# Kernel tuning notes

Measured on AMD Instinct MI355X. Metric: run time of the kernel, lower is better.

## Reference

```python
import jax, jax.numpy as jnp
import numpy as np

H = 32          # num_attention_heads
ROPE_BASE = 10000.0


def _rotary_freqs_cis(seq_len: int, head_dim: int) -> jnp.ndarray:
    # complex e^{i * pos * theta_j}, shape [seq_len, head_dim//2]
    inv_freq = 1.0 / (ROPE_BASE ** (jnp.arange(0, head_dim, 2, dtype=jnp.float32) / head_dim))
    angles = jnp.arange(seq_len, dtype=jnp.float32)[:, None] * inv_freq[None, :]
    return jax.lax.complex(jnp.cos(angles), jnp.sin(angles))


def _apply_rotary(u: jnp.ndarray, freqs_cis: jnp.ndarray) -> jnp.ndarray:
    # u: [B, S, H, hd]; faithful to apply_rotary_emb (interleaved pairs -> complex mul)
    ur = u.astype(jnp.float32).reshape(*u.shape[:-1], -1, 2)
    uc = jax.lax.complex(ur[..., 0], ur[..., 1])
    # freqs_cis broadcast: [1, S, 1, hd//2]
    uc = uc * freqs_cis[None, :, None, :]
    return jnp.stack((jnp.real(uc), jnp.imag(uc)), axis=-1).reshape(u.shape)


def setup_inputs() -> dict:
    key = jax.random.key(0)
    ks = jax.random.split(key, 5)
    B, S, D = 1, 2048, 4096
    init_std = 0.02
    x = jax.random.normal(ks[0], (B, S, D), dtype=jnp.float32)
    wq = jax.random.normal(ks[1], (D, D), dtype=jnp.float32) * init_std
    wk = jax.random.normal(ks[2], (D, D), dtype=jnp.float32) * init_std
    wv = jax.random.normal(ks[3], (D, D), dtype=jnp.float32) * init_std
    wo = jax.random.normal(ks[4], (D, D), dtype=jnp.float32) * init_std
    return {"x": x, "wq": wq, "wk": wk, "wv": wv, "wo": wo}


def reference(x, wq, wk, wv, wo):
    B, S, D = x.shape
    hd = D // H  # head_dim = 128
    q = (x @ wq).reshape(B, S, H, hd)
    k = (x @ wk).reshape(B, S, H, hd)
    v = (x @ wv).reshape(B, S, H, hd)

    freqs_cis = _rotary_freqs_cis(S, hd)
    q = _apply_rotary(q, freqs_cis)
    k = _apply_rotary(k, freqs_cis)
    # n_rep == 1 (num_key_value_heads == num_attention_heads) -> repeat_kv is identity

    scale = 1.0 / jnp.sqrt(jnp.float32(hd))
    scores = jnp.einsum('bqhd,bkhd->bhqk', q, k) * scale  # [B, H, S, S]
    causal = jnp.tril(jnp.ones((S, S), dtype=bool))
    neg = jnp.finfo(scores.dtype).min
    scores = jnp.where(causal[None, None, :, :], scores, neg)
    probs = jax.nn.softmax(scores, axis=-1)
    attn = jnp.einsum('bhqk,bkhd->bqhd', probs, v).reshape(B, S, D)
    return attn @ wo
```

## Files before the change

kernel.cpp:

```cpp
#include <hip/hip_runtime.h>
#include <stdint.h>

#define S_LEN 2048
#define DMODEL 4096
#define NHEAD 32
#define HDIM 128

typedef __attribute__((ext_vector_type(8))) short bf16x8;
typedef __attribute__((ext_vector_type(4))) float f32x4;

__device__ __forceinline__ unsigned short f2bf(float f) {
    union { float f; unsigned u; } v; v.f = f;
    unsigned u = v.u;
    unsigned r = (u + 0x7FFFu + ((u >> 16) & 1u)) >> 16;
    return (unsigned short)r;
}
__device__ __forceinline__ float bf2f(unsigned short h) {
    union { unsigned u; float f; } v; v.u = ((unsigned)h) << 16;
    return v.f;
}

__global__ void convert_x_kernel(const float* __restrict__ x,
                                 unsigned short* __restrict__ xb, int n4) {
    int t = blockIdx.x * blockDim.x + threadIdx.x;
    if (t >= n4) return;
    float4 v = ((const float4*)x)[t];
    ushort4 o;
    o.x = f2bf(v.x); o.y = f2bf(v.y); o.z = f2bf(v.z); o.w = f2bf(v.w);
    ((ushort4*)xb)[t] = o;
}

__global__ void convert_wt_kernel(const float* __restrict__ w,
                                  unsigned short* __restrict__ wt) {
    __shared__ unsigned short t[64][65];
    int n0 = blockIdx.x * 64, k0 = blockIdx.y * 64;
    for (int i = 0; i < 16; ++i) {
        int o = threadIdx.x + i * 256;
        int r = o >> 6, c = o & 63;
        t[r][c] = f2bf(w[(size_t)(k0 + r) * DMODEL + n0 + c]);
    }
    __syncthreads();
    for (int i = 0; i < 16; ++i) {
        int o = threadIdx.x + i * 256;
        int rr = o >> 6, kk = o & 63;
        wt[(size_t)(n0 + rr) * DMODEL + k0 + kk] = t[kk][rr];
    }
}


#define MFMA16(a, b, c) __builtin_amdgcn_mfma_f32_16x16x32_bf16(a, b, c, 0, 0, 0)

#define GLDS(g, l) __builtin_amdgcn_global_load_lds( \
    (__attribute__((address_space(1))) unsigned int*)(g), \
    (__attribute__((address_space(3))) unsigned int*)(l), 16, 0, 0)

#define VMCNT_(n) asm volatile("s_waitcnt vmcnt(" #n ")" ::: "memory")
#define VMCNT(n) VMCNT_(n)

#define PH_SYNC() \
    __builtin_amdgcn_sched_barrier(0); \
    __builtin_amdgcn_s_barrier(); \
    asm volatile("s_waitcnt lgkmcnt(0)" ::: "memory"); \
    __builtin_amdgcn_sched_barrier(0)

#define PH_END() \
    __builtin_amdgcn_s_setprio(0); \
    __builtin_amdgcn_sched_barrier(0); \
    __builtin_amdgcn_s_barrier(); \
    __builtin_amdgcn_sched_barrier(0)

#define PH_END_VM(VM) \
    __builtin_amdgcn_s_setprio(0); \
    __builtin_amdgcn_sched_barrier(0); \
    VMCNT(VM); \
    __builtin_amdgcn_s_barrier(); \
    __builtin_amdgcn_sched_barrier(0)

#define STAGE_A(T, PAR, J) do { \
    size_t ko_ = (size_t)(T) * 64 + (J) * 32; \
    GLDS(gA0 + ko_, As + ((PAR) * 2 + (J)) * 8192 + w * 512); \
    GLDS(gA1 + ko_, As + ((PAR) * 2 + (J)) * 8192 + 4096 + w * 512); \
} while (0)
#define STAGE_B(T, PAR, J) do { \
    size_t ko_ = (size_t)(T) * 64 + (J) * 32; \
    GLDS(gB + ko_, Bs + ((PAR) * 2 + (J)) * 4096 + w * 512); \
} while (0)

#define TILE(T, P, S1, S2, VM2, VM4) do { \
    const unsigned short* AsT = As + (P) * 16384; \
    const unsigned short* BsT = Bs + (P) * 8192; \
    bf16x8 af0, af1, af2, af3, bf0, bf1, bf2, bf3; \
    af0 = *(const bf16x8*)&AsT[offA0]; \
    af1 = *(const bf16x8*)&AsT[offA1]; \
    af2 = *(const bf16x8*)&AsT[offA2]; \
    af3 = *(const bf16x8*)&AsT[offA3]; \
    bf0 = *(const bf16x8*)&BsT[offB0]; \
    bf1 = *(const bf16x8*)&BsT[offB1]; \
    if (S1) STAGE_A((T) + 1, (P) ^ 1, 1); \
    PH_SYNC(); \
    __builtin_amdgcn_s_setprio(1); \
    acc[0][0] = MFMA16(af0, bf0, acc[0][0]); \
    acc[1][0] = MFMA16(af1, bf0, acc[1][0]); \
    acc[2][0] = MFMA16(af2, bf0, acc[2][0]); \
    acc[3][0] = MFMA16(af3, bf0, acc[3][0]); \
    acc[0][1] = MFMA16(af0, bf1, acc[0][1]); \
    acc[1][1] = MFMA16(af1, bf1, acc[1][1]); \
    acc[2][1] = MFMA16(af2, bf1, acc[2][1]); \
    acc[3][1] = MFMA16(af3, bf1, acc[3][1]); \
    PH_END(); \
    bf2 = *(const bf16x8*)&BsT[offB2]; \
    bf3 = *(const bf16x8*)&BsT[offB3]; \
    if (S1) STAGE_B((T) + 1, (P) ^ 1, 1); \
    PH_SYNC(); \
    __builtin_amdgcn_s_setprio(1); \
    acc[0][2] = MFMA16(af0, bf2, acc[0][2]); \
    acc[1][2] = MFMA16(af1, bf2, acc[1][2]); \
    acc[2][2] = MFMA16(af2, bf2, acc[2][2]); \
    acc[3][2] = MFMA16(af3, bf2, acc[3][2]); \
    acc[0][3] = MFMA16(af0, bf3, acc[0][3]); \
    acc[1][3] = MFMA16(af1, bf3, acc[1][3]); \
    acc[2][3] = MFMA16(af2, bf3, acc[2][3]); \
    acc[3][3] = MFMA16(af3, bf3, acc[3][3]); \
    PH_END_VM(VM2); \
    af0 = *(const bf16x8*)&AsT[8192 + offA0]; \
    af1 = *(const bf16x8*)&AsT[8192 + offA1]; \
    af2 = *(const bf16x8*)&AsT[8192 + offA2]; \
    af3 = *(const bf16x8*)&AsT[8192 + offA3]; \
    bf0 = *(const bf16x8*)&BsT[4096 + offB0]; \
    bf1 = *(const bf16x8*)&BsT[4096 + offB1]; \
    if (S2) STAGE_A((T) + 2, (P), 0); \
    PH_SYNC(); \
    __builtin_amdgcn_s_setprio(1); \
    acc[0][0] = MFMA16(af0, bf0, acc[0][0]); \
    acc[1][0] = MFMA16(af1, bf0, acc[1][0]); \
    acc[2][0] = MFMA16(af2, bf0, acc[2][0]); \
    acc[3][0] = MFMA16(af3, bf0, acc[3][0]); \
    acc[0][1] = MFMA16(af0, bf1, acc[0][1]); \
    acc[1][1] = MFMA16(af1, bf1, acc[1][1]); \
    acc[2][1] = MFMA16(af2, bf1, acc[2][1]); \
    acc[3][1] = MFMA16(af3, bf1, acc[3][1]); \
    PH_END(); \
    bf2 = *(const bf16x8*)&BsT[4096 + offB2]; \
    bf3 = *(const bf16x8*)&BsT[4096 + offB3]; \
    if (S2) STAGE_B((T) + 2, (P), 0); \
    PH_SYNC(); \
    __builtin_amdgcn_s_setprio(1); \
    acc[0][2] = MFMA16(af0, bf2, acc[0][2]); \
    acc[1][2] = MFMA16(af1, bf2, acc[1][2]); \
    acc[2][2] = MFMA16(af2, bf2, acc[2][2]); \
    acc[3][2] = MFMA16(af3, bf2, acc[3][2]); \
    acc[0][3] = MFMA16(af0, bf3, acc[0][3]); \
    acc[1][3] = MFMA16(af1, bf3, acc[1][3]); \
    acc[2][3] = MFMA16(af2, bf3, acc[2][3]); \
    acc[3][3] = MFMA16(af3, bf3, acc[3][3]); \
    PH_END_VM(VM4); \
} while (0)

template<int STORE_MODE>
__global__ __launch_bounds__(512, 2)
void gemm8p_kernel(const unsigned short* __restrict__ A,
                   const unsigned short* __restrict__ BT,
                   void* __restrict__ C) {
    constexpr int M = S_LEN, N = DMODEL, K = DMODEL;
    constexpr int NT = K / 64;
    extern __shared__ __align__(16) unsigned short sm[];
    unsigned short* As = sm;
    unsigned short* Bs = sm + 32768;

    const int tid = threadIdx.x;
    const int lane = tid & 63;
    const int w = tid >> 6;
    const int wr = w >> 1, wc = w & 1;
    const int q = lane >> 4, lm = lane & 15;

    int orig = blockIdx.y * gridDim.x + blockIdx.x;
    const int by = orig & 7;
    const int bx = orig >> 3;
    const int m0 = by * 256, n0 = bx * 128;

    const int c4 = tid & 3, r4 = tid >> 2, s4 = (tid >> 3) & 3;
    const unsigned short* gA0 = A + (size_t)(m0 + r4) * K + ((c4 ^ s4) * 8);
    const unsigned short* gA1 = gA0 + (size_t)128 * K;
    const unsigned short* gB  = BT + (size_t)(n0 + r4) * K + ((c4 ^ s4) * 8);

#define FRAGOFF(r_) ((r_) * 32 + ((q ^ (((r_) >> 1) & 3)) * 8))
    const int rA = wr * 64 + lm, rB = wc * 64 + lm;
    const int offA0 = FRAGOFF(rA);
    const int offA1 = FRAGOFF(rA + 16);
    const int offA2 = FRAGOFF(rA + 32);
    const int offA3 = FRAGOFF(rA + 48);
    const int offB0 = FRAGOFF(rB);
    const int offB1 = FRAGOFF(rB + 16);
    const int offB2 = FRAGOFF(rB + 32);
    const int offB3 = FRAGOFF(rB + 48);
#undef FRAGOFF

    f32x4 zero = {0.f, 0.f, 0.f, 0.f};
    f32x4 acc[4][4];
    for (int i = 0; i < 4; ++i)
        for (int j = 0; j < 4; ++j) acc[i][j] = zero;

    STAGE_A(0, 0, 0); STAGE_B(0, 0, 0);
    STAGE_A(0, 0, 1); STAGE_B(0, 0, 1);
    STAGE_A(1, 1, 0); STAGE_B(1, 1, 0);
    VMCNT(6);
    __builtin_amdgcn_s_barrier();
    __builtin_amdgcn_sched_barrier(0);

    for (int t = 0; t < NT - 2; t += 2) {
        TILE(t, 0, true, true, 6, 6);
        TILE(t + 1, 1, true, true, 6, 6);
    }
    TILE(NT - 2, 0, true, false, 6, 3);
    TILE(NT - 1, 1, false, false, 0, 0);

    for (int mi = 0; mi < 4; ++mi) {
        int mbase = m0 + wr * 64 + mi * 16 + q * 4;
        for (int ni = 0; ni < 4; ++ni) {
            int n = n0 + wc * 64 + ni * 16 + lm;
            if (STORE_MODE == 0) {
                unsigned short* Cb = (unsigned short*)C;
                for (int r = 0; r < 4; ++r)
                    Cb[(size_t)(mbase + r) * N + n] = f2bf(acc[mi][ni][r]);
            } else if (STORE_MODE == 1) {
                unsigned short* Cb = (unsigned short*)C;
                ushort4 v;
                v.x = f2bf(acc[mi][ni][0]); v.y = f2bf(acc[mi][ni][1]);
                v.z = f2bf(acc[mi][ni][2]); v.w = f2bf(acc[mi][ni][3]);
                *(ushort4*)&Cb[(size_t)n * M + mbase] = v;
            } else {
                float* Cf = (float*)C;
                for (int r = 0; r < 4; ++r)
                    Cf[(size_t)(mbase + r) * N + n] = acc[mi][ni][r];
            }
        }
    }
}

__global__ void rope_kernel(unsigned short* __restrict__ qb,
                            unsigned short* __restrict__ kb) {
    int t = blockIdx.x * blockDim.x + threadIdx.x;
    if (t >= S_LEN * DMODEL / 2) return;
    int s = t >> 11;
    int p = t & 2047;
    int j = p & 63;
    float ang = (float)s * exp2f((float)j * -0.2076205059304602f);
    float sn, cs;
    sincosf(ang, &sn, &cs);
    size_t idx = (size_t)s * DMODEL + 2 * p;
    const float SC = 0.08838834764831845f;
    float a0 = bf2f(qb[idx]), a1 = bf2f(qb[idx + 1]);
    qb[idx]     = f2bf((a0 * cs - a1 * sn) * SC);
    qb[idx + 1] = f2bf((a0 * sn + a1 * cs) * SC);
    float b0 = bf2f(kb[idx]), b1 = bf2f(kb[idx + 1]);
    kb[idx]     = f2bf(b0 * cs - b1 * sn);
    kb[idx + 1] = f2bf(b0 * sn + b1 * cs);
}

__global__ __launch_bounds__(256, 2)
void attn_kernel(const unsigned short* __restrict__ qb,
                 const unsigned short* __restrict__ kb,
                 const unsigned short* __restrict__ vt,
                 unsigned short* __restrict__ ab) {
    __shared__ __align__(16) unsigned short Ks[64 * 128];
    __shared__ __align__(16) unsigned short VTs[128 * 64];
    __shared__ __align__(16) unsigned short Pb[4][32 * 72];
    const int t = threadIdx.x;
    const int lane = t & 63;
    const int w = t >> 6;
    const int h = blockIdx.y;
    const int q0 = ((int)gridDim.x - 1 - (int)blockIdx.x) * 128;
    const int qw = q0 + w * 32;
    const int q = lane >> 4, lm = lane & 15;

    const int krow = t >> 2;
    const int kcol = t & 3;
    const int vrow = t >> 1;
    const int vcol = t & 1;

    const unsigned short* gK = kb + (size_t)krow * DMODEL + h * HDIM;
    const unsigned short* gV = vt + (size_t)(h * HDIM + vrow) * S_LEN;

    bf16x8 qf[2][4];
#pragma unroll
    for (int qt = 0; qt < 2; ++qt)
#pragma unroll
        for (int kc = 0; kc < 4; ++kc)
            qf[qt][kc] = *(const bf16x8*)&qb[(size_t)(qw + qt * 16 + lm) * DMODEL
                                            + h * HDIM + kc * 32 + q * 8];

    f32x4 zero = {0.f, 0.f, 0.f, 0.f};
    f32x4 o[2][8];
#pragma unroll
    for (int qt = 0; qt < 2; ++qt)
        for (int i = 0; i < 8; ++i) o[qt][i] = zero;
    float mrow[2][4], lrow[2][4];
#pragma unroll
    for (int qt = 0; qt < 2; ++qt)
        for (int r = 0; r < 4; ++r) { mrow[qt][r] = -1e30f; lrow[qt][r] = 0.f; }

    const int nch = q0 / 64 + 2;

    bf16x8 kreg[4], vreg[4];
#pragma unroll
    for (int i = 0; i < 4; ++i) {
        kreg[i] = *(const bf16x8*)&gK[(size_t)0 * DMODEL + (kcol + i * 4) * 8];
        vreg[i] = *(const bf16x8*)&gV[0 + (vcol + i * 2) * 8];
    }
#pragma unroll
    for (int i = 0; i < 4; ++i) {
        *(bf16x8*)&Ks[krow * 128 + (((kcol + i * 4) ^ (krow & 15)) * 8)] = kreg[i];
        *(bf16x8*)&VTs[vrow * 64 + (((vcol + i * 2) ^ (vrow & 7)) * 8)] = vreg[i];
    }
    __syncthreads();

    for (int c = 0; c < nch; ++c) {
        const int j0 = c * 64;
        if (c + 1 < nch) {
            const size_t jn = (size_t)(j0 + 64);
#pragma unroll
            for (int i = 0; i < 4; ++i) {
                kreg[i] = *(const bf16x8*)&gK[jn * DMODEL + (kcol + i * 4) * 8];
                vreg[i] = *(const bf16x8*)&gV[jn + (vcol + i * 2) * 8];
            }
        }

        if (j0 <= qw + 31) {
            f32x4 s[2][4];
#pragma unroll
            for (int qt = 0; qt < 2; ++qt)
                for (int ks = 0; ks < 4; ++ks) s[qt][ks] = zero;
#pragma unroll
            for (int kc = 0; kc < 4; ++kc)
#pragma unroll
                for (int ks = 0; ks < 4; ++ks) {
                    bf16x8 kf = *(const bf16x8*)&Ks[(ks * 16 + lm) * 128
                                                    + (((kc * 4 + q) ^ lm) * 8)];
                    s[0][ks] = __builtin_amdgcn_mfma_f32_16x16x32_bf16(qf[0][kc], kf, s[0][ks], 0, 0, 0);
                    s[1][ks] = __builtin_amdgcn_mfma_f32_16x16x32_bf16(qf[1][kc], kf, s[1][ks], 0, 0, 0);
                }
            if (j0 + 63 > qw) {
#pragma unroll
                for (int qt = 0; qt < 2; ++qt)
#pragma unroll
                    for (int ks = 0; ks < 4; ++ks)
#pragma unroll
                        for (int r = 0; r < 4; ++r)
                            if (j0 + ks * 16 + lm > qw + qt * 16 + q * 4 + r)
                                s[qt][ks][r] = -1e30f;
            }

            float mx[2][4];
#pragma unroll
            for (int qt = 0; qt < 2; ++qt)
#pragma unroll
                for (int r = 0; r < 4; ++r)
                    mx[qt][r] = fmaxf(fmaxf(s[qt][0][r], s[qt][1][r]),
                                      fmaxf(s[qt][2][r], s[qt][3][r]));
#pragma unroll
            for (int st = 1; st <= 8; st <<= 1)
#pragma unroll
                for (int qt = 0; qt < 2; ++qt)
#pragma unroll
                    for (int r = 0; r < 4; ++r)
                        mx[qt][r] = fmaxf(mx[qt][r], __shfl_xor(mx[qt][r], st));

            float aln[2][4], mnv[2][4], rs[2][4];
#pragma unroll
            for (int qt = 0; qt < 2; ++qt)
#pragma unroll
                for (int r = 0; r < 4; ++r) {
                    mnv[qt][r] = fmaxf(mrow[qt][r], mx[qt][r]);
                    aln[qt][r] = __expf(mrow[qt][r] - mnv[qt][r]);
                    mrow[qt][r] = mnv[qt][r];
                }
#pragma unroll
            for (int qt = 0; qt < 2; ++qt)
#pragma unroll
                for (int ks = 0; ks < 4; ++ks)
#pragma unroll
                    for (int r = 0; r < 4; ++r)
                        s[qt][ks][r] = __expf(s[qt][ks][r] - mnv[qt][r]);
#pragma unroll
            for (int qt = 0; qt < 2; ++qt)
#pragma unroll
                for (int r = 0; r < 4; ++r)
                    rs[qt][r] = (s[qt][0][r] + s[qt][1][r]) + (s[qt][2][r] + s[qt][3][r]);
#pragma unroll
            for (int st = 1; st <= 8; st <<= 1)
#pragma unroll
                for (int qt = 0; qt < 2; ++qt)
#pragma unroll
                    for (int r = 0; r < 4; ++r)
                        rs[qt][r] += __shfl_xor(rs[qt][r], st);
#pragma unroll
            for (int qt = 0; qt < 2; ++qt)
#pragma unroll
                for (int r = 0; r < 4; ++r)
                    lrow[qt][r] = lrow[qt][r] * aln[qt][r] + rs[qt][r];

#pragma unroll
            for (int qt = 0; qt < 2; ++qt)
#pragma unroll
                for (int ks = 0; ks < 4; ++ks)
#pragma unroll
                    for (int r = 0; r < 4; ++r)
                        Pb[w][(qt * 16 + q * 4 + r) * 72 + ks * 16 + lm] = f2bf(s[qt][ks][r]);

            bf16x8 pA[2][2];
#pragma unroll
            for (int qt = 0; qt < 2; ++qt) {
                pA[qt][0] = *(const bf16x8*)&Pb[w][(qt * 16 + lm) * 72 + q * 8];
                pA[qt][1] = *(const bf16x8*)&Pb[w][(qt * 16 + lm) * 72 + 32 + q * 8];
            }
#pragma unroll
            for (int nt = 0; nt < 8; ++nt) {
                int d = nt * 16 + lm;
                bf16x8 vf0 = *(const bf16x8*)&VTs[d * 64 + ((q ^ (d & 7)) * 8)];
                bf16x8 vf1 = *(const bf16x8*)&VTs[d * 64 + (((4 + q) ^ (d & 7)) * 8)];
#pragma unroll
                for (int qt = 0; qt < 2; ++qt) {
                    f32x4 oo = o[qt][nt];
#pragma unroll
                    for (int r = 0; r < 4; ++r) oo[r] *= aln[qt][r];
                    oo = __builtin_amdgcn_mfma_f32_16x16x32_bf16(pA[qt][0], vf0, oo, 0, 0, 0);
                    o[qt][nt] = __builtin_amdgcn_mfma_f32_16x16x32_bf16(pA[qt][1], vf1, oo, 0, 0, 0);
                }
            }
        }

        __syncthreads();
        if (c + 1 < nch) {
#pragma unroll
            for (int i = 0; i < 4; ++i) {
                *(bf16x8*)&Ks[krow * 128 + (((kcol + i * 4) ^ (krow & 15)) * 8)] = kreg[i];
                *(bf16x8*)&VTs[vrow * 64 + (((vcol + i * 2) ^ (vrow & 7)) * 8)] = vreg[i];
            }
        }
        __syncthreads();
    }

    float inv[2][4];
#pragma unroll
    for (int qt = 0; qt < 2; ++qt)
#pragma unroll
        for (int r = 0; r < 4; ++r) inv[qt][r] = 1.0f / lrow[qt][r];
#pragma unroll
    for (int qt = 0; qt < 2; ++qt)
#pragma unroll
        for (int nt = 0; nt < 8; ++nt) {
            int d = h * HDIM + lm + nt * 16;
#pragma unroll
            for (int r = 0; r < 4; ++r)
                ab[(size_t)(qw + qt * 16 + q * 4 + r) * DMODEL + d] =
                    f2bf(o[qt][nt][r] * inv[qt][r]);
        }
}

extern "C" void kernel_launch(void* const* d_in, const int* in_sizes, int n_in,
                              void* d_out, int out_size, void* d_ws, size_t ws_size,
                              hipStream_t stream) {
    const float* x  = (const float*)d_in[0];
    const float* wq = (const float*)d_in[1];
    const float* wk = (const float*)d_in[2];
    const float* wv = (const float*)d_in[3];
    const float* wo = (const float*)d_in[4];
    char* ws = (char*)d_ws;
    const size_t MB = 1024 * 1024;
    unsigned short* xb  = (unsigned short*)(ws + 0 * MB);
    unsigned short* qb  = (unsigned short*)(ws + 16 * MB);
    unsigned short* kb  = (unsigned short*)(ws + 32 * MB);
    unsigned short* vtb = (unsigned short*)(ws + 48 * MB);
    unsigned short* ab  = (unsigned short*)(ws + 64 * MB);
    unsigned short* wtb = (unsigned short*)(ws + 80 * MB);

    static int attr_done = 0;
    if (!attr_done) {
        hipFuncSetAttribute((const void*)&gemm8p_kernel<0>,
                            hipFuncAttributeMaxDynamicSharedMemorySize, 98304);
        hipFuncSetAttribute((const void*)&gemm8p_kernel<1>,
                            hipFuncAttributeMaxDynamicSharedMemorySize, 98304);
        hipFuncSetAttribute((const void*)&gemm8p_kernel<2>,
                            hipFuncAttributeMaxDynamicSharedMemorySize, 98304);
        attr_done = 1;
    }

    dim3 cg(64, 64);
    dim3 gg(32, 8);

    convert_x_kernel<<<(S_LEN * DMODEL / 4) / 256, 256, 0, stream>>>(x, xb, S_LEN * DMODEL / 4);

    convert_wt_kernel<<<cg, 256, 0, stream>>>(wq, wtb);
    gemm8p_kernel<0><<<gg, 512, 98304, stream>>>(xb, wtb, qb);
    convert_wt_kernel<<<cg, 256, 0, stream>>>(wk, wtb);
    gemm8p_kernel<0><<<gg, 512, 98304, stream>>>(xb, wtb, kb);
    convert_wt_kernel<<<cg, 256, 0, stream>>>(wv, wtb);
    gemm8p_kernel<1><<<gg, 512, 98304, stream>>>(xb, wtb, vtb);

    rope_kernel<<<(S_LEN * DMODEL / 2) / 256, 256, 0, stream>>>(qb, kb);

    attn_kernel<<<dim3(S_LEN / 128, NHEAD), 256, 0, stream>>>(qb, kb, vtb, ab);

    convert_wt_kernel<<<cg, 256, 0, stream>>>(wo, wtb);
    gemm8p_kernel<2><<<gg, 512, 98304, stream>>>(ab, wtb, d_out);
}
```

Before: 721.9 us.

## Restructure attention inner loop with async K staging and register-shuffled P

The attention kernel now double-buffers K tiles in shared memory, filled with direct global-to-LDS loads (GLDS) so the next tile streams in while the current one is computed, and one barrier per chunk replaces the two __syncthreads. V is read straight from global memory into registers instead of going through LDS. The QK^T MFMA operands are swapped so each lane holds a transposed score tile, which makes row max and row sum reductions need only two cross-lane shuffles. P is packed to bf16 with v_cvt_pk_bf16_f32 and rearranged into MFMA operand layout with lane shuffles instead of an LDS round trip. The cost is more shuffle traffic and uncached global V loads issued on every chunk.

New measurement: 744.1 us. 3.1% more time.

```diff
diff --git a/kernel.cpp b/kernel.cpp
--- a/kernel.cpp
+++ b/kernel.cpp
@@ -262,9 +262,7 @@
                  const unsigned short* __restrict__ kb,
                  const unsigned short* __restrict__ vt,
                  unsigned short* __restrict__ ab) {
-    __shared__ __align__(16) unsigned short Ks[64 * 128];
-    __shared__ __align__(16) unsigned short VTs[128 * 64];
-    __shared__ __align__(16) unsigned short Pb[4][32 * 72];
+    __shared__ __align__(16) unsigned short Ks[2][64 * 128];
     const int t = threadIdx.x;
     const int lane = t & 63;
     const int w = t >> 6;
@@ -272,14 +270,18 @@
     const int q0 = ((int)gridDim.x - 1 - (int)blockIdx.x) * 128;
     const int qw = q0 + w * 32;
     const int q = lane >> 4, lm = lane & 15;
-
-    const int krow = t >> 2;
-    const int kcol = t & 3;
-    const int vrow = t >> 1;
-    const int vcol = t & 1;
-
-    const unsigned short* gK = kb + (size_t)krow * DMODEL + h * HDIM;
-    const unsigned short* gV = vt + (size_t)(h * HDIM + vrow) * S_LEN;
+    const int w16 = w * 16;
+
+#define ATT_STAGE(CHUNK, BUF) do { \
+    size_t rbase_ = (size_t)((CHUNK) * 64); \
+    _Pragma("unroll") \
+    for (int j_ = 0; j_ < 4; ++j_) { \
+        int rloc_ = w16 + j_ * 4 + (lane >> 4); \
+        const unsigned short* src_ = kb + (rbase_ + rloc_) * DMODEL + h * HDIM \
+                                     + (((lane & 15) ^ (rloc_ & 15)) * 8); \
+        GLDS(src_, &Ks[BUF][(w16 + j_ * 4) * 128]); \
+    } \
+} while (0)
 
     bf16x8 qf[2][4];
 #pragma unroll
@@ -294,38 +296,31 @@
 #pragma unroll
     for (int qt = 0; qt < 2; ++qt)
         for (int i = 0; i < 8; ++i) o[qt][i] = zero;
-    float mrow[2][4], lrow[2][4];
-#pragma unroll
-    for (int qt = 0; qt < 2; ++qt)
-        for (int r = 0; r < 4; ++r) { mrow[qt][r] = -1e30f; lrow[qt][r] = 0.f; }
+    float mrow[2] = {-1e30f, -1e30f};
+    float lrow[2] = {0.f, 0.f};
 
     const int nch = q0 / 64 + 2;
 
-    bf16x8 kreg[4], vreg[4];
-#pragma unroll
-    for (int i = 0; i < 4; ++i) {
-        kreg[i] = *(const bf16x8*)&gK[(size_t)0 * DMODEL + (kcol + i * 4) * 8];
-        vreg[i] = *(const bf16x8*)&gV[0 + (vcol + i * 2) * 8];
-    }
-#pragma unroll
-    for (int i = 0; i < 4; ++i) {
-        *(bf16x8*)&Ks[krow * 128 + (((kcol + i * 4) ^ (krow & 15)) * 8)] = kreg[i];
-        *(bf16x8*)&VTs[vrow * 64 + (((vcol + i * 2) ^ (vrow & 7)) * 8)] = vreg[i];
-    }
-    __syncthreads();
+    ATT_STAGE(0, 0);
+    VMCNT(0);
+    __builtin_amdgcn_s_barrier();
+    __builtin_amdgcn_sched_barrier(0);
 
     for (int c = 0; c < nch; ++c) {
         const int j0 = c * 64;
-        if (c + 1 < nch) {
-            const size_t jn = (size_t)(j0 + 64);
-#pragma unroll
-            for (int i = 0; i < 4; ++i) {
-                kreg[i] = *(const bf16x8*)&gK[jn * DMODEL + (kcol + i * 4) * 8];
-                vreg[i] = *(const bf16x8*)&gV[jn + (vcol + i * 2) * 8];
+        const int p = c & 1;
+        if (c + 1 < nch) ATT_STAGE(c + 1, p ^ 1);
+
+        if (j0 <= qw + 31) {
+            bf16x8 vf0[8], vf1[8];
+#pragma unroll
+            for (int nt = 0; nt < 8; ++nt) {
+                const unsigned short* gv = vt + (size_t)(h * HDIM + nt * 16 + lm) * S_LEN
+                                           + j0 + q * 8;
+                vf0[nt] = *(const bf16x8*)gv;
+                vf1[nt] = *(const bf16x8*)(gv + 32);
             }
-        }
-
-        if (j0 <= qw + 31) {
+
             f32x4 s[2][4];
 #pragma unroll
             for (int qt = 0; qt < 2; ++qt)
@@ -334,10 +329,10 @@
             for (int kc = 0; kc < 4; ++kc)
 #pragma unroll
                 for (int ks = 0; ks < 4; ++ks) {
-                    bf16x8 kf = *(const bf16x8*)&Ks[(ks * 16 + lm) * 128
-                                                    + (((kc * 4 + q) ^ lm) * 8)];
-                    s[0][ks] = __builtin_amdgcn_mfma_f32_16x16x32_bf16(qf[0][kc], kf, s[0][ks], 0, 0, 0);
-                    s[1][ks] = __builtin_amdgcn_mfma_f32_16x16x32_bf16(qf[1][kc], kf, s[1][ks], 0, 0, 0);
+                    bf16x8 kf = *(const bf16x8*)&Ks[p][(ks * 16 + lm) * 128
+                                                      + (((kc * 4 + q) ^ lm) * 8)];
+                    s[0][ks] = __builtin_amdgcn_mfma_f32_16x16x32_bf16(kf, qf[0][kc], s[0][ks], 0, 0, 0);
+                    s[1][ks] = __builtin_amdgcn_mfma_f32_16x16x32_bf16(kf, qf[1][kc], s[1][ks], 0, 0, 0);
                 }
             if (j0 + 63 > qw) {
 #pragma unroll
@@ -346,105 +341,108 @@
                     for (int ks = 0; ks < 4; ++ks)
 #pragma unroll
                         for (int r = 0; r < 4; ++r)
-                            if (j0 + ks * 16 + lm > qw + qt * 16 + q * 4 + r)
+                            if (j0 + ks * 16 + q * 4 + r > qw + qt * 16 + lm)
                                 s[qt][ks][r] = -1e30f;
             }
 
-            float mx[2][4];
+            float alnv[2];
+#pragma unroll
+            for (int qt = 0; qt < 2; ++qt) {
+                float m01 = fmaxf(fmaxf(s[qt][0][0], s[qt][0][1]), fmaxf(s[qt][0][2], s[qt][0][3]));
+                float m11 = fmaxf(fmaxf(s[qt][1][0], s[qt][1][1]), fmaxf(s[qt][1][2], s[qt][1][3]));
+                float m21 = fmaxf(fmaxf(s[qt][2][0], s[qt][2][1]), fmaxf(s[qt][2][2], s[qt][2][3]));
+                float m31 = fmaxf(fmaxf(s[qt][3][0], s[qt][3][1]), fmaxf(s[qt][3][2], s[qt][3][3]));
+                float mloc = fmaxf(fmaxf(m01, m11), fmaxf(m21, m31));
+                mloc = fmaxf(mloc, __shfl_xor(mloc, 16));
+                mloc = fmaxf(mloc, __shfl_xor(mloc, 32));
+                float mn = fmaxf(mrow[qt], mloc);
+                alnv[qt] = __expf(mrow[qt] - mn);
+                mrow[qt] = mn;
+#pragma unroll
+                for (int ks = 0; ks < 4; ++ks)
+#pragma unroll
+                    for (int r = 0; r < 4; ++r)
+                        s[qt][ks][r] = __expf(s[qt][ks][r] - mn);
+                float r0 = (s[qt][0][0] + s[qt][0][1]) + (s[qt][0][2] + s[qt][0][3]);
+                float r1 = (s[qt][1][0] + s[qt][1][1]) + (s[qt][1][2] + s[qt][1][3]);
+                float r2 = (s[qt][2][0] + s[qt][2][1]) + (s[qt][2][2] + s[qt][2][3]);
+                float r3 = (s[qt][3][0] + s[qt][3][1]) + (s[qt][3][2] + s[qt][3][3]);
+                float rloc = (r0 + r1) + (r2 + r3);
+                rloc += __shfl_xor(rloc, 16);
+                rloc += __shfl_xor(rloc, 32);
+                lrow[qt] = lrow[qt] * alnv[qt] + rloc;
+            }
+
+            unsigned Wd[2][4][2];
 #pragma unroll
             for (int qt = 0; qt < 2; ++qt)
 #pragma unroll
+                for (int ks = 0; ks < 4; ++ks)
+#pragma unroll
+                    for (int u = 0; u < 2; ++u) {
+                        unsigned wv;
+                        asm("v_cvt_pk_bf16_f32 %0, %1, %2"
+                            : "=v"(wv) : "v"(s[qt][ks][2 * u]), "v"(s[qt][ks][2 * u + 1]));
+                        Wd[qt][ks][u] = wv;
+                    }
+
+            union U8 { bf16x8 v; unsigned u[4]; };
+            const int sA = ((lane >> 4) & 1) * 32 + lm;
+            const int sB = sA + 16;
+            const bool hi2 = (lane & 32) != 0;
+            U8 pA[2][2];
+#pragma unroll
+            for (int qt = 0; qt < 2; ++qt)
+#pragma unroll
+                for (int hh = 0; hh < 2; ++hh) {
+                    unsigned a0 = __shfl((int)Wd[qt][2 * hh][0], sA);
+                    unsigned b0 = __shfl((int)Wd[qt][2 * hh + 1][0], sA);
+                    pA[qt][hh].u[0] = hi2 ? b0 : a0;
+                    unsigned a1 = __shfl((int)Wd[qt][2 * hh][1], sA);
+                    unsigned b1 = __shfl((int)Wd[qt][2 * hh + 1][1], sA);
+                    pA[qt][hh].u[1] = hi2 ? b1 : a1;
+                    unsigned a2 = __shfl((int)Wd[qt][2 * hh][0], sB);
+                    unsigned b2 = __shfl((int)Wd[qt][2 * hh + 1][0], sB);
+                    pA[qt][hh].u[2] = hi2 ? b2 : a2;
+                    unsigned a3 = __shfl((int)Wd[qt][2 * hh][1], sB);
+                    unsigned b3 = __shfl((int)Wd[qt][2 * hh + 1][1], sB);
+                    pA[qt][hh].u[3] = hi2 ? b3 : a3;
+                }
+
+            float alno[2][4];
+#pragma unroll
+            for (int qt = 0; qt < 2; ++qt)
+#pragma unroll
                 for (int r = 0; r < 4; ++r)
-                    mx[qt][r] = fmaxf(fmaxf(s[qt][0][r], s[qt][1][r]),
-                                      fmaxf(s[qt][2][r], s[qt][3][r]));
-#pragma unroll
-            for (int st = 1; st <= 8; st <<= 1)
-#pragma unroll
-                for (int qt = 0; qt < 2; ++qt)
-#pragma unroll
-                    for (int r = 0; r < 4; ++r)
-                        mx[qt][r] = fmaxf(mx[qt][r], __shfl_xor(mx[qt][r], st));
-
-            float aln[2][4], mnv[2][4], rs[2][4];
-#pragma unroll
-            for (int qt = 0; qt < 2; ++qt)
-#pragma unroll
-                for (int r = 0; r < 4; ++r) {
-                    mnv[qt][r] = fmaxf(mrow[qt][r], mx[qt][r]);
-                    aln[qt][r] = __expf(mrow[qt][r] - mnv[qt][r]);
-                    mrow[qt][r] = mnv[qt][r];
-                }
-#pragma unroll
-            for (int qt = 0; qt < 2; ++qt)
-#pragma unroll
-                for (int ks = 0; ks < 4; ++ks)
-#pragma unroll
-                    for (int r = 0; r < 4; ++r)
-                        s[qt][ks][r] = __expf(s[qt][ks][r] - mnv[qt][r]);
-#pragma unroll
-            for (int qt = 0; qt < 2; ++qt)
-#pragma unroll
-                for (int r = 0; r < 4; ++r)
-                    rs[qt][r] = (s[qt][0][r] + s[qt][1][r]) + (s[qt][2][r] + s[qt][3][r]);
-#pragma unroll
-            for (int st = 1; st <= 8; st <<= 1)
-#pragma unroll
-                for (int qt = 0; qt < 2; ++qt)
-#pragma unroll
-                    for (int r = 0; r < 4; ++r)
-                        rs[qt][r] += __shfl_xor(rs[qt][r], st);
-#pragma unroll
-            for (int qt = 0; qt < 2; ++qt)
-#pragma unroll
-                for (int r = 0; r < 4; ++r)
-                    lrow[qt][r] = lrow[qt][r] * aln[qt][r] + rs[qt][r];
-
-#pragma unroll
-            for (int qt = 0; qt < 2; ++qt)
-#pragma unroll
-                for (int ks = 0; ks < 4; ++ks)
-#pragma unroll
-                    for (int r = 0; r < 4; ++r)
-                        Pb[w][(qt * 16 + q * 4 + r) * 72 + ks * 16 + lm] = f2bf(s[qt][ks][r]);
-
-            bf16x8 pA[2][2];
-#pragma unroll
-            for (int qt = 0; qt < 2; ++qt) {
-                pA[qt][0] = *(const bf16x8*)&Pb[w][(qt * 16 + lm) * 72 + q * 8];
-                pA[qt][1] = *(const bf16x8*)&Pb[w][(qt * 16 + lm) * 72 + 32 + q * 8];
-            }
+                    alno[qt][r] = __shfl(alnv[qt], (lane >> 4) * 4 + r);
+
 #pragma unroll
             for (int nt = 0; nt < 8; ++nt) {
-                int d = nt * 16 + lm;
-                bf16x8 vf0 = *(const bf16x8*)&VTs[d * 64 + ((q ^ (d & 7)) * 8)];
-                bf16x8 vf1 = *(const bf16x8*)&VTs[d * 64 + (((4 + q) ^ (d & 7)) * 8)];
 #pragma unroll
                 for (int qt = 0; qt < 2; ++qt) {
                     f32x4 oo = o[qt][nt];
 #pragma unroll
-                    for (int r = 0; r < 4; ++r) oo[r] *= aln[qt][r];
-                    oo = __builtin_amdgcn_mfma_f32_16x16x32_bf16(pA[qt][0], vf0, oo, 0, 0, 0);
-                    o[qt][nt] = __builtin_amdgcn_mfma_f32_16x16x32_bf16(pA[qt][1], vf1, oo, 0, 0, 0);
+                    for (int r = 0; r < 4; ++r) oo[r] *= alno[qt][r];
+                    oo = __builtin_amdgcn_mfma_f32_16x16x32_bf16(pA[qt][0].v, vf0[nt], oo, 0, 0, 0);
+                    o[qt][nt] = __builtin_amdgcn_mfma_f32_16x16x32_bf16(pA[qt][1].v, vf1[nt], oo, 0, 0, 0);
                 }
             }
         }
 
-        __syncthreads();
-        if (c + 1 < nch) {
-#pragma unroll
-            for (int i = 0; i < 4; ++i) {
-                *(bf16x8*)&Ks[krow * 128 + (((kcol + i * 4) ^ (krow & 15)) * 8)] = kreg[i];
-                *(bf16x8*)&VTs[vrow * 64 + (((vcol + i * 2) ^ (vrow & 7)) * 8)] = vreg[i];
-            }
-        }
-        __syncthreads();
-    }
-
-    float inv[2][4];
-#pragma unroll
-    for (int qt = 0; qt < 2; ++qt)
-#pragma unroll
-        for (int r = 0; r < 4; ++r) inv[qt][r] = 1.0f / lrow[qt][r];
+        __builtin_amdgcn_sched_barrier(0);
+        VMCNT(0);
+        __builtin_amdgcn_s_barrier();
+        __builtin_amdgcn_sched_barrier(0);
+    }
+
+    float invo[2][4];
+#pragma unroll
+    for (int qt = 0; qt < 2; ++qt) {
+        float iv = 1.0f / lrow[qt];
+#pragma unroll
+        for (int r = 0; r < 4; ++r)
+            invo[qt][r] = __shfl(iv, (lane >> 4) * 4 + r);
+    }
 #pragma unroll
     for (int qt = 0; qt < 2; ++qt)
 #pragma unroll
@@ -453,8 +451,9 @@
 #pragma unroll
             for (int r = 0; r < 4; ++r)
                 ab[(size_t)(qw + qt * 16 + q * 4 + r) * DMODEL + d] =
-                    f2bf(o[qt][nt][r] * inv[qt][r]);
+                    f2bf(o[qt][nt][r] * invo[qt][r]);
         }
+#undef ATT_STAGE
 }
 
 extern "C" void kernel_launch(void* const* d_in, const int* in_sizes, int n_in,
```
